# Kernel tuning notes

Measured on AMD Instinct MI355X. Metric: run time of the kernel, lower is better.

The kernel has to match this reference:

```python
import jax, jax.numpy as jnp
import numpy as np

B, S, E = 2, 2048, 1024
N_HEADS = 16
HEAD_DIM = E // N_HEADS  # 64
ATTN_SCALE = 1.0 / np.sqrt(E)  # NOTE: original scales by 1/sqrt(hidden_dim_phi), not head_dim
ROPE_BASE = 10000.0


def _rope(t):
    # t: (B, H, S, D) with D = HEAD_DIM; interleaved-pair RoPE (torchtune-style)
    d = t.shape[-1]
    s = t.shape[-2]
    inv_freq = 1.0 / (ROPE_BASE ** (jnp.arange(0, d, 2, dtype=jnp.float32) / d))  # (D/2,)
    ang = jnp.arange(s, dtype=jnp.float32)[:, None] * inv_freq[None, :]  # (S, D/2)
    cos, sin = jnp.cos(ang), jnp.sin(ang)  # (S, D/2)
    tp = t.reshape(t.shape[:-1] + (d // 2, 2))
    te, to = tp[..., 0], tp[..., 1]  # (B,H,S,D/2)
    oe = te * cos - to * sin
    oo = te * sin + to * cos
    return jnp.stack([oe, oo], axis=-1).reshape(t.shape)


def setup_inputs() -> dict:
    key = jax.random.key(0)
    ks = jax.random.split(key, 5)
    std = 0.02
    return {
        "x": jax.random.normal(ks[0], (B, S, E), dtype=jnp.float32),
        "W_q": jax.random.normal(ks[1], (E, E), dtype=jnp.float32) * std,
        "W_k": jax.random.normal(ks[2], (E, E), dtype=jnp.float32) * std,
        "W_v": jax.random.normal(ks[3], (E, E), dtype=jnp.float32) * std,
        "W_o": jax.random.normal(ks[4], (E, E), dtype=jnp.float32) * std,
    }


def reference(x, W_q, W_k, W_v, W_o):
    b, s, e = x.shape
    hd = e // N_HEADS
    # projections -> (B, H, S, D)
    def proj(w):
        return (x @ w).reshape(b, s, N_HEADS, hd).transpose(0, 2, 1, 3)
    q = _rope(proj(W_q))
    k = _rope(proj(W_k))
    v = proj(W_v)
    scores = jnp.einsum('bhsd,bhtd->bhst', q, k) * ATTN_SCALE  # (B,H,S,S)
    causal = jnp.triu(jnp.ones((s, s), dtype=bool), k=1)
    scores = jnp.where(causal, -jnp.inf, scores)
    probs = jax.nn.softmax(scores, axis=-1)  # dropout is identity in eval mode
    out = jnp.einsum('bhst,bhtd->bhsd', probs, v)
    out = out.transpose(0, 2, 1, 3).reshape(b, s, e)
    return out @ W_o
```

## Files before the change

kernel.cpp:

```cpp
#include <hip/hip_runtime.h>
#include <hip/hip_bf16.h>

#define S_LEN 2048
#define E_DIM 1024
#define NH 16
#define HD 64
#define ATTN_SCALE 0.03125f
#define QSCALE_L2E 0.045084312f

typedef __attribute__((ext_vector_type(8))) short short8;
typedef __attribute__((ext_vector_type(8))) unsigned short ushort8;
typedef __attribute__((ext_vector_type(4))) unsigned short ushort4_t;
typedef __attribute__((ext_vector_type(4))) float f32x4;
typedef __attribute__((ext_vector_type(4))) float f4;
typedef __attribute__((ext_vector_type(2))) unsigned int uint2_t;

__device__ __forceinline__ float bf2f(unsigned short u) {
    unsigned int x = ((unsigned int)u) << 16;
    return __builtin_bit_cast(float, x);
}
__device__ __forceinline__ unsigned short f2bf(float f) {
    unsigned int x = __builtin_bit_cast(unsigned int, f);
    x += 0x7FFFu + ((x >> 16) & 1u);
    return (unsigned short)(x >> 16);
}
__device__ __forceinline__ void gload16(const unsigned short* g, unsigned short* l) {
    __builtin_amdgcn_global_load_lds(
        (__attribute__((address_space(1))) void*)g,
        (__attribute__((address_space(3))) void*)l, 16, 0, 0);
}

__global__ __launch_bounds__(256) void k_convert(const float* __restrict__ x,
                                                 unsigned short* __restrict__ xb) {
    size_t i = ((size_t)blockIdx.x * 256 + threadIdx.x) * 8;
    f4 a = *(const f4*)(x + i);
    f4 b = *(const f4*)(x + i + 4);
    ushort8 o;
    o[0] = f2bf(a[0]); o[1] = f2bf(a[1]); o[2] = f2bf(a[2]); o[3] = f2bf(a[3]);
    o[4] = f2bf(b[0]); o[5] = f2bf(b[1]); o[6] = f2bf(b[2]); o[7] = f2bf(b[3]);
    *(ushort8*)(xb + i) = o;
}

__global__ __launch_bounds__(256) void k_transw(const float* W0, const float* W1,
                                                const float* W2, const float* W3,
                                                unsigned short* T0, unsigned short* T1,
                                                unsigned short* T2, unsigned short* T3) {
    const float* W; unsigned short* T;
    switch (blockIdx.z) {
        case 0: W = W0; T = T0; break;
        case 1: W = W1; T = T1; break;
        case 2: W = W2; T = T2; break;
        default: W = W3; T = T3; break;
    }
    __shared__ float tile[32][33];
    int tx = threadIdx.x, ty = threadIdx.y;
    int bx = blockIdx.x * 32, by = blockIdx.y * 32;
#pragma unroll
    for (int i = 0; i < 4; i++)
        tile[ty + i * 8][tx] = W[(size_t)(by + ty + i * 8) * E_DIM + bx + tx];
    __syncthreads();
#pragma unroll
    for (int i = 0; i < 4; i++)
        T[(size_t)(bx + ty + i * 8) * E_DIM + by + tx] = f2bf(tile[tx][ty + i * 8]);
}

__global__ __launch_bounds__(256) void k_rope_table(float* __restrict__ cosT,
                                                    float* __restrict__ sinT) {
    int idx = blockIdx.x * 256 + threadIdx.x;
    int s = idx >> 5, j = idx & 31;
    float inv = expf(-(float)j * (9.210340371976184f / 32.f));
    float ang = (float)s * inv;
    cosT[idx] = cosf(ang);
    sinT[idx] = sinf(ang);
}

template <int BM, int BN, int NBN, bool QKV3>
__global__ __launch_bounds__(256, 3)
void k_gemmN(const unsigned short* __restrict__ A,
             const unsigned short* __restrict__ B,
             unsigned short* __restrict__ Qo,
             unsigned short* __restrict__ Ko,
             unsigned short* __restrict__ Vto,
             float* __restrict__ Fo,
             const float* __restrict__ cosT,
             const float* __restrict__ sinT) {
    constexpr int THREADS = 256;
    constexpr int WM = BM / 2, WN = BN / 2;
    constexpr int FM = WM / 16, FN = WN / 16;
    constexpr int NT = E_DIM / 64;
    constexpr int AR = BM * 8 / THREADS;
    constexpr int BR = BN * 8 / THREADS;
    constexpr int STG = AR + BR;
    constexpr int NWG = (4096 / BM) * NBN;
    __shared__ unsigned short Al[2][BM * 64];
    __shared__ unsigned short Bl[2][BN * 64];
    int tid = threadIdx.x, lane = tid & 63, wid = tid >> 6;
    int l15 = lane & 15, lg = lane >> 4;
    int wr = wid >> 1, wc = wid & 1;
    int orig = blockIdx.y * NBN + blockIdx.x;
    int wg = (orig & 7) * (NWG / 8) + (orig >> 3);
    int bm = wg / NBN, bn = wg % NBN;

    auto stage = [&](int buf, int k0) {
#pragma unroll
        for (int i = 0; i < AR; i++) {
            int r = i * (THREADS / 8) + wid * 8 + (lane >> 3);
            int cs = (lane & 7) ^ (r & 7);
            gload16(A + (size_t)(bm * BM + r) * E_DIM + k0 + cs * 8,
                    &Al[buf][i * (THREADS * 8) + wid * 512]);
        }
#pragma unroll
        for (int i = 0; i < BR; i++) {
            int r = i * (THREADS / 8) + wid * 8 + (lane >> 3);
            int cs = (lane & 7) ^ (r & 7);
            gload16(B + (size_t)(bn * BN + r) * E_DIM + k0 + cs * 8,
                    &Bl[buf][i * (THREADS * 8) + wid * 512]);
        }
    };

    f32x4 acc[FM][FN] = {};
    stage(0, 0);
    for (int t = 0; t < NT; t++) {
        int cur = t & 1;
        if (t + 1 < NT) {
            stage(cur ^ 1, (t + 1) * 64);
            asm volatile("s_waitcnt vmcnt(%0)" :: "n"(STG) : "memory");
        } else {
            asm volatile("s_waitcnt vmcnt(0)" ::: "memory");
        }
        __builtin_amdgcn_s_barrier();
        __builtin_amdgcn_sched_barrier(0);
#pragma unroll
        for (int ks = 0; ks < 2; ks++) {
            short8 af[FM], bfv[FN];
#pragma unroll
            for (int m = 0; m < FM; m++) {
                int r = wr * WM + m * 16 + l15;
                int gc = ks * 4 + lg;
                af[m] = *(const short8*)&Al[cur][r * 64 + ((gc ^ (r & 7)) << 3)];
            }
#pragma unroll
            for (int n = 0; n < FN; n++) {
                int r = wc * WN + n * 16 + l15;
                int gc = ks * 4 + lg;
                bfv[n] = *(const short8*)&Bl[cur][r * 64 + ((gc ^ (r & 7)) << 3)];
            }
            __builtin_amdgcn_s_setprio(1);
#pragma unroll
            for (int m = 0; m < FM; m++)
#pragma unroll
                for (int n = 0; n < FN; n++)
                    acc[m][n] = __builtin_amdgcn_mfma_f32_16x16x32_bf16(
                        af[m], bfv[n], acc[m][n], 0, 0, 0);
            __builtin_amdgcn_s_setprio(0);
        }
        __builtin_amdgcn_s_barrier();
    }
#pragma unroll
    for (int m = 0; m < FM; m++) {
        int r0 = bm * BM + wr * WM + m * 16 + lg * 4;
#pragma unroll
        for (int n = 0; n < FN; n++) {
            int colg = bn * BN + wc * WN + n * 16 + l15;
            if (QKV3) {
                int z = colg >> 10, c1 = colg & 1023;
                if (z == 2) {
                    int h = c1 >> 6, d = c1 & 63;
                    int bb = r0 >> 11, s = r0 & 2047;
                    ushort4_t p;
#pragma unroll
                    for (int r = 0; r < 4; r++) p[r] = f2bf(acc[m][n][r]);
                    *(ushort4_t*)(Vto + (((size_t)((bb * 16 + h) * 64 + d)) << 11) + s) = p;
                } else {
                    unsigned short* T = z ? Ko : Qo;
                    int dl = c1 & 63, j = dl >> 1;
                    float sgn = (dl & 1) ? 1.f : -1.f;
                    float scq = z ? 1.f : QSCALE_L2E;
#pragma unroll
                    for (int r = 0; r < 4; r++) {
                        int row = r0 + r, s = row & 2047;
                        float c = cosT[s * 32 + j], sn = sinT[s * 32 + j];
                        float v = acc[m][n][r];
                        float p = __shfl_xor(v, 1);
                        T[(size_t)row * E_DIM + c1] = f2bf((v * c + sgn * p * sn) * scq);
                    }
                }
            } else {
#pragma unroll
                for (int r = 0; r < 4; r++)
                    Fo[(size_t)(r0 + r) * E_DIM + colg] = acc[m][n][r];
            }
        }
    }
}

__global__ __launch_bounds__(256, 3) void k_attn(const unsigned short* __restrict__ Q,
                                                 const unsigned short* __restrict__ K,
                                                 const unsigned short* __restrict__ Vt,
                                                 unsigned short* __restrict__ O) {
    __shared__ unsigned short K_lds[2][64 * 64];
    __shared__ unsigned short V_lds[2][64 * 64];
    __shared__ unsigned short P_lds[4][16][72];
    int tid = threadIdx.x, lane = tid & 63, wid = tid >> 6;
    int l15 = lane & 15, lg = lane >> 4;
    int orig = blockIdx.y * 16 + blockIdx.x;
    int wg = (orig & 7) * 64 + (orig >> 3);
    int jp = wg & 15, bh = wg >> 4;
    int b = bh >> 4, h = bh & 15;
    const size_t base_qk = (size_t)b * S_LEN * E_DIM + (size_t)h * HD;
    const unsigned short* Vbh = Vt + ((size_t)(bh * 64) << 11);

    auto stageK = [&](int buf, int kt) {
#pragma unroll
        for (int i = 0; i < 2; i++) {
            int r = i * 32 + (tid >> 3);
            int cs = (tid & 7) ^ (r & 7);
            gload16(K + base_qk + (size_t)(kt * 64 + r) * E_DIM + cs * 8,
                    &K_lds[buf][i * 2048 + tid * 8]);
        }
    };
    auto stageV = [&](int buf, int kt) {
#pragma unroll
        for (int i = 0; i < 2; i++) {
            int r = i * 32 + (tid >> 3);
            int cs = (tid & 7) ^ (r & 7);
            gload16(Vbh + (size_t)r * 2048 + kt * 64 + cs * 8,
                    &V_lds[buf][i * 2048 + tid * 8]);
        }
    };

    for (int pass = 0; pass < 2; ++pass) {
        int qt = pass ? (31 - jp) : jp;
        const unsigned short* Qb = Q + base_qk + (size_t)(qt * 64 + wid * 16) * E_DIM;
        short8 bq[2];
#pragma unroll
        for (int s2 = 0; s2 < 2; s2++)
            bq[s2] = *(const short8*)(Qb + (size_t)l15 * E_DIM + s2 * 32 + lg * 8);
        f32x4 acc_o[4] = {};
        float m_i = -1e30f, l_i = 0.f;
        int q_glob = qt * 64 + wid * 16 + l15;
        int nkt = qt + 1;
        stageK(0, 0);
        stageV(0, 0);
        asm volatile("s_waitcnt vmcnt(0)" ::: "memory");
        __builtin_amdgcn_s_barrier();
        __builtin_amdgcn_sched_barrier(0);
        int cur = 0;
        for (int kt = 0; kt < nkt; ++kt) {
            if (kt + 1 < nkt) {
                stageK(cur ^ 1, kt + 1);
                stageV(cur ^ 1, kt + 1);
            }
            f32x4 acc_s[4] = {};
            __builtin_amdgcn_s_setprio(1);
#pragma unroll
            for (int mf = 0; mf < 4; mf++) {
                int rK = mf * 16 + l15;
#pragma unroll
                for (int s2 = 0; s2 < 2; s2++) {
                    int gc = s2 * 4 + lg;
                    short8 a = *(const short8*)
                        &K_lds[cur][rK * 64 + ((gc ^ (rK & 7)) << 3)];
                    acc_s[mf] = __builtin_amdgcn_mfma_f32_16x16x32_bf16(
                        a, bq[s2], acc_s[mf], 0, 0, 0);
                }
            }
            __builtin_amdgcn_s_setprio(0);
            float sv[16];
            float vmax = -1e30f;
            if (kt == nkt - 1) {
#pragma unroll
                for (int mf = 0; mf < 4; mf++)
#pragma unroll
                    for (int r = 0; r < 4; r++) {
                        int kg = kt * 64 + mf * 16 + lg * 4 + r;
                        float v = acc_s[mf][r];
                        if (kg > q_glob) v = -1e30f;
                        sv[mf * 4 + r] = v;
                        vmax = fmaxf(vmax, v);
                    }
            } else {
#pragma unroll
                for (int mf = 0; mf < 4; mf++)
#pragma unroll
                    for (int r = 0; r < 4; r++) {
                        float v = acc_s[mf][r];
                        sv[mf * 4 + r] = v;
                        vmax = fmaxf(vmax, v);
                    }
            }
            vmax = fmaxf(vmax, __shfl_xor(vmax, 16));
            vmax = fmaxf(vmax, __shfl_xor(vmax, 32));
            if (!__all(vmax - m_i <= 8.0f)) {
                float m_new = fmaxf(m_i, vmax);
                float corr = exp2f(m_i - m_new);
                l_i *= corr;
#pragma unroll
                for (int r = 0; r < 4; r++) {
                    float c4 = __shfl(corr, lg * 4 + r);
#pragma unroll
                    for (int nf = 0; nf < 4; nf++) acc_o[nf][r] *= c4;
                }
                m_i = m_new;
            }
            float rowsum = 0.f;
#pragma unroll
            for (int i = 0; i < 16; i++) {
                float p = exp2f(sv[i] - m_i);
                sv[i] = p;
                rowsum += p;
            }
            rowsum += __shfl_xor(rowsum, 16);
            rowsum += __shfl_xor(rowsum, 32);
            l_i += rowsum;
#pragma unroll
            for (int mf = 0; mf < 4; mf++) {
                unsigned int w0, w1;
                asm("v_cvt_pk_bf16_f32 %0, %1, %2"
                    : "=v"(w0) : "v"(sv[mf * 4 + 0]), "v"(sv[mf * 4 + 1]));
                asm("v_cvt_pk_bf16_f32 %0, %1, %2"
                    : "=v"(w1) : "v"(sv[mf * 4 + 2]), "v"(sv[mf * 4 + 3]));
                uint2_t w; w[0] = w0; w[1] = w1;
                *(uint2_t*)&P_lds[wid][l15][mf * 16 + lg * 4] = w;
            }
            __builtin_amdgcn_s_setprio(1);
#pragma unroll
            for (int s2 = 0; s2 < 2; s2++) {
                short8 pa = *(const short8*)&P_lds[wid][l15][s2 * 32 + lg * 8];
#pragma unroll
                for (int nf = 0; nf < 4; nf++) {
                    int rV = nf * 16 + l15;
                    int gc = s2 * 4 + lg;
                    short8 bv = *(const short8*)
                        &V_lds[cur][rV * 64 + ((gc ^ (rV & 7)) << 3)];
                    acc_o[nf] = __builtin_amdgcn_mfma_f32_16x16x32_bf16(
                        pa, bv, acc_o[nf], 0, 0, 0);
                }
            }
            __builtin_amdgcn_s_setprio(0);
            asm volatile("s_waitcnt vmcnt(0)" ::: "memory");
            __builtin_amdgcn_s_barrier();
            __builtin_amdgcn_sched_barrier(0);
            cur ^= 1;
        }
        unsigned short* Ob = O + base_qk + (size_t)(qt * 64 + wid * 16) * E_DIM;
#pragma unroll
        for (int r = 0; r < 4; r++) {
            float linv = 1.f / __shfl(l_i, lg * 4 + r);
#pragma unroll
            for (int nf = 0; nf < 4; nf++)
                Ob[(size_t)(lg * 4 + r) * E_DIM + nf * 16 + l15] =
                    f2bf(acc_o[nf][r] * linv);
        }
    }
}

extern "C" void kernel_launch(void* const* d_in, const int* in_sizes, int n_in,
                              void* d_out, int out_size, void* d_ws, size_t ws_size,
                              hipStream_t stream) {
    (void)in_sizes; (void)n_in; (void)out_size; (void)ws_size;
    const float* x  = (const float*)d_in[0];
    const float* Wq = (const float*)d_in[1];
    const float* Wk = (const float*)d_in[2];
    const float* Wv = (const float*)d_in[3];
    const float* Wo = (const float*)d_in[4];

    unsigned short* us = (unsigned short*)d_ws;
    unsigned short* xb    = us;
    unsigned short* WqkvT = us + 4194304;
    unsigned short* WoT   = us + 7340032;
    unsigned short* Qb    = us + 8388608;
    unsigned short* Kb    = us + 12582912;
    unsigned short* Vt    = us + 16777216;
    unsigned short* AO    = us + 20971520;
    float* cosT = (float*)((char*)d_ws + 50331648);
    float* sinT = cosT + 65536;

    k_convert<<<2048, 256, 0, stream>>>(x, xb);
    k_transw<<<dim3(32, 32, 4), dim3(32, 8), 0, stream>>>(
        Wq, Wk, Wv, Wo, WqkvT, WqkvT + 1048576, WqkvT + 2097152, WoT);
    k_rope_table<<<256, 256, 0, stream>>>(cosT, sinT);
    k_gemmN<128, 64, 48, true><<<dim3(48, 32), 256, 0, stream>>>(
        xb, WqkvT, Qb, Kb, Vt, nullptr, cosT, sinT);
    k_attn<<<dim3(16, 32), 256, 0, stream>>>(Qb, Kb, Vt, AO);
    k_gemmN<128, 64, 16, false><<<dim3(16, 32), 256, 0, stream>>>(
        AO, WoT, nullptr, nullptr, nullptr, (float*)d_out, cosT, sinT);
}
```

Measured before the change: 117.5 us.

## Shrink attention blocks to 32 query rows and triple-buffer K/V loads

The attention kernel now uses 128-thread workgroups that each cover 32 query rows per pass, doubling the grid to 1024 blocks so causal work is spread more evenly and more blocks can be resident. K/V staging moves from double to triple buffering, prefetching two tiles ahead with partial vmcnt waits instead of draining all loads every iteration. The trade-off is that each K/V tile is now loaded by half as many threads and reused by fewer query rows, which raises global/L2 traffic per unit of compute, and more LDS is needed per block.

```diff
diff --git a/kernel.cpp b/kernel.cpp
--- a/kernel.cpp
+++ b/kernel.cpp
@@ -194,62 +194,69 @@
     }
 }
 
-__global__ __launch_bounds__(256, 3) void k_attn(const unsigned short* __restrict__ Q,
+__global__ __launch_bounds__(128, 2) void k_attn(const unsigned short* __restrict__ Q,
                                                  const unsigned short* __restrict__ K,
                                                  const unsigned short* __restrict__ Vt,
                                                  unsigned short* __restrict__ O) {
-    __shared__ unsigned short K_lds[2][64 * 64];
-    __shared__ unsigned short V_lds[2][64 * 64];
-    __shared__ unsigned short P_lds[4][16][72];
+    __shared__ unsigned short K_lds[3][64 * 64];
+    __shared__ unsigned short V_lds[3][64 * 64];
+    __shared__ unsigned short P_lds[2][16][72];
     int tid = threadIdx.x, lane = tid & 63, wid = tid >> 6;
     int l15 = lane & 15, lg = lane >> 4;
-    int orig = blockIdx.y * 16 + blockIdx.x;
-    int wg = (orig & 7) * 64 + (orig >> 3);
-    int jp = wg & 15, bh = wg >> 4;
+    int orig = blockIdx.y * 32 + blockIdx.x;
+    int wg = (orig & 7) * 128 + (orig >> 3);
+    int jp = wg & 31, bh = wg >> 5;
     int b = bh >> 4, h = bh & 15;
     const size_t base_qk = (size_t)b * S_LEN * E_DIM + (size_t)h * HD;
     const unsigned short* Vbh = Vt + ((size_t)(bh * 64) << 11);
 
     auto stageK = [&](int buf, int kt) {
 #pragma unroll
-        for (int i = 0; i < 2; i++) {
-            int r = i * 32 + (tid >> 3);
-            int cs = (tid & 7) ^ (r & 7);
+        for (int i = 0; i < 4; i++) {
+            int r = i * 16 + wid * 8 + (lane >> 3);
+            int cs = (lane & 7) ^ (r & 7);
             gload16(K + base_qk + (size_t)(kt * 64 + r) * E_DIM + cs * 8,
-                    &K_lds[buf][i * 2048 + tid * 8]);
+                    &K_lds[buf][i * 1024 + wid * 512]);
         }
     };
     auto stageV = [&](int buf, int kt) {
 #pragma unroll
-        for (int i = 0; i < 2; i++) {
-            int r = i * 32 + (tid >> 3);
-            int cs = (tid & 7) ^ (r & 7);
+        for (int i = 0; i < 4; i++) {
+            int r = i * 16 + wid * 8 + (lane >> 3);
+            int cs = (lane & 7) ^ (r & 7);
             gload16(Vbh + (size_t)r * 2048 + kt * 64 + cs * 8,
-                    &V_lds[buf][i * 2048 + tid * 8]);
+                    &V_lds[buf][i * 1024 + wid * 512]);
         }
     };
 
     for (int pass = 0; pass < 2; ++pass) {
-        int qt = pass ? (31 - jp) : jp;
-        const unsigned short* Qb = Q + base_qk + (size_t)(qt * 64 + wid * 16) * E_DIM;
+        int p = pass ? (63 - jp) : jp;
+        const unsigned short* Qb = Q + base_qk + (size_t)(p * 32 + wid * 16) * E_DIM;
         short8 bq[2];
 #pragma unroll
         for (int s2 = 0; s2 < 2; s2++)
             bq[s2] = *(const short8*)(Qb + (size_t)l15 * E_DIM + s2 * 32 + lg * 8);
         f32x4 acc_o[4] = {};
         float m_i = -1e30f, l_i = 0.f;
-        int q_glob = qt * 64 + wid * 16 + l15;
-        int nkt = qt + 1;
+        int q_glob = p * 32 + wid * 16 + l15;
+        int nkt = (p + 2) >> 1;
+        __builtin_amdgcn_s_barrier();
         stageK(0, 0);
         stageV(0, 0);
-        asm volatile("s_waitcnt vmcnt(0)" ::: "memory");
+        if (nkt > 1) {
+            stageK(1, 1);
+            stageV(1, 1);
+            asm volatile("s_waitcnt vmcnt(8)" ::: "memory");
+        } else {
+            asm volatile("s_waitcnt vmcnt(0)" ::: "memory");
+        }
         __builtin_amdgcn_s_barrier();
         __builtin_amdgcn_sched_barrier(0);
-        int cur = 0;
         for (int kt = 0; kt < nkt; ++kt) {
-            if (kt + 1 < nkt) {
-                stageK(cur ^ 1, kt + 1);
-                stageV(cur ^ 1, kt + 1);
+            int cur = kt % 3;
+            if (kt + 2 < nkt) {
+                stageK((kt + 2) % 3, kt + 2);
+                stageV((kt + 2) % 3, kt + 2);
             }
             f32x4 acc_s[4] = {};
             __builtin_amdgcn_s_setprio(1);
@@ -306,9 +313,9 @@
             float rowsum = 0.f;
 #pragma unroll
             for (int i = 0; i < 16; i++) {
-                float p = exp2f(sv[i] - m_i);
-                sv[i] = p;
-                rowsum += p;
+                float pv = exp2f(sv[i] - m_i);
+                sv[i] = pv;
+                rowsum += pv;
             }
             rowsum += __shfl_xor(rowsum, 16);
             rowsum += __shfl_xor(rowsum, 32);
@@ -338,12 +345,16 @@
                 }
             }
             __builtin_amdgcn_s_setprio(0);
-            asm volatile("s_waitcnt vmcnt(0)" ::: "memory");
-            __builtin_amdgcn_s_barrier();
-            __builtin_amdgcn_sched_barrier(0);
-            cur ^= 1;
-        }
-        unsigned short* Ob = O + base_qk + (size_t)(qt * 64 + wid * 16) * E_DIM;
+            if (kt + 1 < nkt) {
+                if (kt + 2 < nkt)
+                    asm volatile("s_waitcnt vmcnt(8)" ::: "memory");
+                else
+                    asm volatile("s_waitcnt vmcnt(0)" ::: "memory");
+                __builtin_amdgcn_s_barrier();
+                __builtin_amdgcn_sched_barrier(0);
+            }
+        }
+        unsigned short* Ob = O + base_qk + (size_t)(p * 32 + wid * 16) * E_DIM;
 #pragma unroll
         for (int r = 0; r < 4; r++) {
             float linv = 1.f / __shfl(l_i, lg * 4 + r);
@@ -382,7 +393,7 @@
     k_rope_table<<<256, 256, 0, stream>>>(cosT, sinT);
     k_gemmN<128, 64, 48, true><<<dim3(48, 32), 256, 0, stream>>>(
         xb, WqkvT, Qb, Kb, Vt, nullptr, cosT, sinT);
-    k_attn<<<dim3(16, 32), 256, 0, stream>>>(Qb, Kb, Vt, AO);
+    k_attn<<<dim3(32, 32), 128, 0, stream>>>(Qb, Kb, Vt, AO);
     k_gemmN<128, 64, 16, false><<<dim3(16, 32), 256, 0, stream>>>(
         AO, WoT, nullptr, nullptr, nullptr, (float*)d_out, cosT, sinT);
 }
```

Result: slower. 151.1 us (+28.6%).

## Rewrite attention with 32x32 MFMA tiles, register P shuffle, and XCD-aware scheduling

Applied to the files above, without the earlier changes.

The attention kernel now uses 2 waves per block, each owning 32 query rows, and runs 32x32x16 bf16 MFMAs instead of 16x16x32. The P matrix is handed from the S-MFMA layout to the PV-MFMA operand through cross-lane shuffles rather than an LDS round trip. Exp uses raw v_exp_f32 and the conditional rescale skip is dropped. Causal load balancing switches from pairing query tiles inside one block to one tile per block, mapped so each XCD handles a few heads with alternating tile order. Output is staged through LDS so global stores are coalesced. Smaller blocks with one tile each may load balance less evenly and reload K/V more often.

```diff
diff --git a/kernel.cpp b/kernel.cpp
--- a/kernel.cpp
+++ b/kernel.cpp
@@ -12,8 +12,9 @@
 typedef __attribute__((ext_vector_type(8))) unsigned short ushort8;
 typedef __attribute__((ext_vector_type(4))) unsigned short ushort4_t;
 typedef __attribute__((ext_vector_type(4))) float f32x4;
+typedef __attribute__((ext_vector_type(16))) float f32x16;
 typedef __attribute__((ext_vector_type(4))) float f4;
-typedef __attribute__((ext_vector_type(2))) unsigned int uint2_t;
+typedef __attribute__((ext_vector_type(4))) unsigned int uint4v;
 
 __device__ __forceinline__ float bf2f(unsigned short u) {
     unsigned int x = ((unsigned int)u) << 16;
@@ -23,6 +24,11 @@
     unsigned int x = __builtin_bit_cast(unsigned int, f);
     x += 0x7FFFu + ((x >> 16) & 1u);
     return (unsigned short)(x >> 16);
+}
+__device__ __forceinline__ float exp2_fast(float x) {
+    float r;
+    asm("v_exp_f32 %0, %1" : "=v"(r) : "v"(x));
+    return r;
 }
 __device__ __forceinline__ void gload16(const unsigned short* g, unsigned short* l) {
     __builtin_amdgcn_global_load_lds(
@@ -194,164 +200,165 @@
     }
 }
 
-__global__ __launch_bounds__(256, 3) void k_attn(const unsigned short* __restrict__ Q,
-                                                 const unsigned short* __restrict__ K,
-                                                 const unsigned short* __restrict__ Vt,
-                                                 unsigned short* __restrict__ O) {
-    __shared__ unsigned short K_lds[2][64 * 64];
-    __shared__ unsigned short V_lds[2][64 * 64];
-    __shared__ unsigned short P_lds[4][16][72];
+__global__ __launch_bounds__(128, 2)
+void k_attn32(const unsigned short* __restrict__ Q,
+              const unsigned short* __restrict__ K,
+              const unsigned short* __restrict__ Vt,
+              unsigned short* __restrict__ O) {
+    __shared__ unsigned short K_lds[2][4096];
+    __shared__ unsigned short V_lds[2][4096];
     int tid = threadIdx.x, lane = tid & 63, wid = tid >> 6;
-    int l15 = lane & 15, lg = lane >> 4;
-    int orig = blockIdx.y * 16 + blockIdx.x;
-    int wg = (orig & 7) * 64 + (orig >> 3);
-    int jp = wg & 15, bh = wg >> 4;
+    int l31 = lane & 31, hi = lane >> 5;
+    int orig = blockIdx.y * 32 + blockIdx.x;
+    int xcd = orig & 7, idx = orig >> 3;
+    int u = idx & 31, v = idx >> 5;
+    int bh = xcd * 4 + v;
+    int p = (v & 1) ? (31 - u) : u;
     int b = bh >> 4, h = bh & 15;
     const size_t base_qk = (size_t)b * S_LEN * E_DIM + (size_t)h * HD;
     const unsigned short* Vbh = Vt + ((size_t)(bh * 64) << 11);
 
     auto stageK = [&](int buf, int kt) {
 #pragma unroll
-        for (int i = 0; i < 2; i++) {
-            int r = i * 32 + (tid >> 3);
+        for (int i = 0; i < 4; i++) {
+            int r = i * 16 + (tid >> 3);
             int cs = (tid & 7) ^ (r & 7);
             gload16(K + base_qk + (size_t)(kt * 64 + r) * E_DIM + cs * 8,
-                    &K_lds[buf][i * 2048 + tid * 8]);
+                    &K_lds[buf][i * 1024 + tid * 8]);
         }
     };
     auto stageV = [&](int buf, int kt) {
 #pragma unroll
-        for (int i = 0; i < 2; i++) {
-            int r = i * 32 + (tid >> 3);
+        for (int i = 0; i < 4; i++) {
+            int r = i * 16 + (tid >> 3);
             int cs = (tid & 7) ^ (r & 7);
             gload16(Vbh + (size_t)r * 2048 + kt * 64 + cs * 8,
-                    &V_lds[buf][i * 2048 + tid * 8]);
+                    &V_lds[buf][i * 1024 + tid * 8]);
         }
     };
 
-    for (int pass = 0; pass < 2; ++pass) {
-        int qt = pass ? (31 - jp) : jp;
-        const unsigned short* Qb = Q + base_qk + (size_t)(qt * 64 + wid * 16) * E_DIM;
-        short8 bq[2];
-#pragma unroll
-        for (int s2 = 0; s2 < 2; s2++)
-            bq[s2] = *(const short8*)(Qb + (size_t)l15 * E_DIM + s2 * 32 + lg * 8);
-        f32x4 acc_o[4] = {};
-        float m_i = -1e30f, l_i = 0.f;
-        int q_glob = qt * 64 + wid * 16 + l15;
-        int nkt = qt + 1;
-        stageK(0, 0);
-        stageV(0, 0);
+    int q_glob = p * 64 + wid * 32 + l31;
+    const unsigned short* Qb = Q + base_qk + (size_t)q_glob * E_DIM;
+    short8 qf[4];
+#pragma unroll
+    for (int s = 0; s < 4; s++)
+        qf[s] = *(const short8*)(Qb + s * 16 + hi * 8);
+
+    f32x16 ot0 = {}, ot1 = {};
+    float m_i = -1e30f, l_i = 0.f;
+    int nkt = p + 1;
+    int swz = l31 & 7;
+    stageK(0, 0);
+    stageV(0, 0);
+    asm volatile("s_waitcnt vmcnt(0)" ::: "memory");
+    __builtin_amdgcn_s_barrier();
+    __builtin_amdgcn_sched_barrier(0);
+    int cur = 0;
+    for (int kt = 0; kt < nkt; ++kt) {
+        if (kt + 1 < nkt) {
+            stageK(cur ^ 1, kt + 1);
+            stageV(cur ^ 1, kt + 1);
+        }
+        f32x16 st0 = {}, st1 = {};
+        __builtin_amdgcn_s_setprio(1);
+#pragma unroll
+        for (int s = 0; s < 4; s++) {
+            int c = ((s * 2 + hi) ^ swz) << 3;
+            short8 ka0 = *(const short8*)&K_lds[cur][l31 * 64 + c];
+            short8 ka1 = *(const short8*)&K_lds[cur][(32 + l31) * 64 + c];
+            st0 = __builtin_amdgcn_mfma_f32_32x32x16_bf16(ka0, qf[s], st0, 0, 0, 0);
+            st1 = __builtin_amdgcn_mfma_f32_32x32x16_bf16(ka1, qf[s], st1, 0, 0, 0);
+        }
+        __builtin_amdgcn_s_setprio(0);
+        float p0[16], p1[16];
+        float vmax = -1e30f;
+        if (kt == nkt - 1) {
+#pragma unroll
+            for (int r = 0; r < 16; r++) {
+                int kg = kt * 64 + (r & 3) + 8 * (r >> 2) + 4 * hi;
+                float v0 = (kg > q_glob) ? -1e30f : st0[r];
+                float v1 = (kg + 32 > q_glob) ? -1e30f : st1[r];
+                p0[r] = v0; p1[r] = v1;
+                vmax = fmaxf(vmax, fmaxf(v0, v1));
+            }
+        } else {
+#pragma unroll
+            for (int r = 0; r < 16; r++) {
+                p0[r] = st0[r]; p1[r] = st1[r];
+                vmax = fmaxf(vmax, fmaxf(st0[r], st1[r]));
+            }
+        }
+        vmax = fmaxf(vmax, __shfl_xor(vmax, 32));
+        float m_new = fmaxf(m_i, vmax);
+        float corr = exp2_fast(m_i - m_new);
+        float rs = 0.f;
+#pragma unroll
+        for (int r = 0; r < 16; r++) {
+            p0[r] = exp2_fast(p0[r] - m_new);
+            p1[r] = exp2_fast(p1[r] - m_new);
+            rs += p0[r] + p1[r];
+        }
+        rs += __shfl_xor(rs, 32);
+        l_i = l_i * corr + rs;
+        m_i = m_new;
+#pragma unroll
+        for (int r = 0; r < 16; r++) { ot0[r] *= corr; ot1[r] *= corr; }
+        unsigned int pk0[8], pk1[8];
+#pragma unroll
+        for (int i = 0; i < 8; i++) {
+            asm("v_cvt_pk_bf16_f32 %0, %1, %2"
+                : "=v"(pk0[i]) : "v"(p0[2 * i]), "v"(p0[2 * i + 1]));
+            asm("v_cvt_pk_bf16_f32 %0, %1, %2"
+                : "=v"(pk1[i]) : "v"(p1[2 * i]), "v"(p1[2 * i + 1]));
+        }
+        bool ishi = hi != 0;
+        __builtin_amdgcn_s_setprio(1);
+#pragma unroll
+        for (int kk = 0; kk < 4; kk++) {
+            const unsigned int* pkt = (kk & 2) ? pk1 : pk0;
+            int off = (kk & 1) * 4;
+            unsigned int a  = pkt[off + 0], b2 = pkt[off + 1];
+            unsigned int c2 = pkt[off + 2], d2 = pkt[off + 3];
+            unsigned int sa = __shfl_xor(a, 32),  sb = __shfl_xor(b2, 32);
+            unsigned int sc = __shfl_xor(c2, 32), sd = __shfl_xor(d2, 32);
+            uint4v w;
+            w[0] = ishi ? sc : a;  w[1] = ishi ? sd : b2;
+            w[2] = ishi ? c2 : sa; w[3] = ishi ? d2 : sb;
+            short8 pf = __builtin_bit_cast(short8, w);
+            int cv = ((kk * 2 + hi) ^ swz) << 3;
+            short8 va0 = *(const short8*)&V_lds[cur][l31 * 64 + cv];
+            short8 va1 = *(const short8*)&V_lds[cur][(32 + l31) * 64 + cv];
+            ot0 = __builtin_amdgcn_mfma_f32_32x32x16_bf16(va0, pf, ot0, 0, 0, 0);
+            ot1 = __builtin_amdgcn_mfma_f32_32x32x16_bf16(va1, pf, ot1, 0, 0, 0);
+        }
+        __builtin_amdgcn_s_setprio(0);
         asm volatile("s_waitcnt vmcnt(0)" ::: "memory");
         __builtin_amdgcn_s_barrier();
         __builtin_amdgcn_sched_barrier(0);
-        int cur = 0;
-        for (int kt = 0; kt < nkt; ++kt) {
-            if (kt + 1 < nkt) {
-                stageK(cur ^ 1, kt + 1);
-                stageV(cur ^ 1, kt + 1);
-            }
-            f32x4 acc_s[4] = {};
-            __builtin_amdgcn_s_setprio(1);
-#pragma unroll
-            for (int mf = 0; mf < 4; mf++) {
-                int rK = mf * 16 + l15;
-#pragma unroll
-                for (int s2 = 0; s2 < 2; s2++) {
-                    int gc = s2 * 4 + lg;
-                    short8 a = *(const short8*)
-                        &K_lds[cur][rK * 64 + ((gc ^ (rK & 7)) << 3)];
-                    acc_s[mf] = __builtin_amdgcn_mfma_f32_16x16x32_bf16(
-                        a, bq[s2], acc_s[mf], 0, 0, 0);
-                }
-            }
-            __builtin_amdgcn_s_setprio(0);
-            float sv[16];
-            float vmax = -1e30f;
-            if (kt == nkt - 1) {
-#pragma unroll
-                for (int mf = 0; mf < 4; mf++)
-#pragma unroll
-                    for (int r = 0; r < 4; r++) {
-                        int kg = kt * 64 + mf * 16 + lg * 4 + r;
-                        float v = acc_s[mf][r];
-                        if (kg > q_glob) v = -1e30f;
-                        sv[mf * 4 + r] = v;
-                        vmax = fmaxf(vmax, v);
-                    }
-            } else {
-#pragma unroll
-                for (int mf = 0; mf < 4; mf++)
-#pragma unroll
-                    for (int r = 0; r < 4; r++) {
-                        float v = acc_s[mf][r];
-                        sv[mf * 4 + r] = v;
-                        vmax = fmaxf(vmax, v);
-                    }
-            }
-            vmax = fmaxf(vmax, __shfl_xor(vmax, 16));
-            vmax = fmaxf(vmax, __shfl_xor(vmax, 32));
-            if (!__all(vmax - m_i <= 8.0f)) {
-                float m_new = fmaxf(m_i, vmax);
-                float corr = exp2f(m_i - m_new);
-                l_i *= corr;
-#pragma unroll
-                for (int r = 0; r < 4; r++) {
-                    float c4 = __shfl(corr, lg * 4 + r);
-#pragma unroll
-                    for (int nf = 0; nf < 4; nf++) acc_o[nf][r] *= c4;
-                }
-                m_i = m_new;
-            }
-            float rowsum = 0.f;
-#pragma unroll
-            for (int i = 0; i < 16; i++) {
-                float p = exp2f(sv[i] - m_i);
-                sv[i] = p;
-                rowsum += p;
-            }
-            rowsum += __shfl_xor(rowsum, 16);
-            rowsum += __shfl_xor(rowsum, 32);
-            l_i += rowsum;
-#pragma unroll
-            for (int mf = 0; mf < 4; mf++) {
-                unsigned int w0, w1;
-                asm("v_cvt_pk_bf16_f32 %0, %1, %2"
-                    : "=v"(w0) : "v"(sv[mf * 4 + 0]), "v"(sv[mf * 4 + 1]));
-                asm("v_cvt_pk_bf16_f32 %0, %1, %2"
-                    : "=v"(w1) : "v"(sv[mf * 4 + 2]), "v"(sv[mf * 4 + 3]));
-                uint2_t w; w[0] = w0; w[1] = w1;
-                *(uint2_t*)&P_lds[wid][l15][mf * 16 + lg * 4] = w;
-            }
-            __builtin_amdgcn_s_setprio(1);
-#pragma unroll
-            for (int s2 = 0; s2 < 2; s2++) {
-                short8 pa = *(const short8*)&P_lds[wid][l15][s2 * 32 + lg * 8];
-#pragma unroll
-                for (int nf = 0; nf < 4; nf++) {
-                    int rV = nf * 16 + l15;
-                    int gc = s2 * 4 + lg;
-                    short8 bv = *(const short8*)
-                        &V_lds[cur][rV * 64 + ((gc ^ (rV & 7)) << 3)];
-                    acc_o[nf] = __builtin_amdgcn_mfma_f32_16x16x32_bf16(
-                        pa, bv, acc_o[nf], 0, 0, 0);
-                }
-            }
-            __builtin_amdgcn_s_setprio(0);
-            asm volatile("s_waitcnt vmcnt(0)" ::: "memory");
-            __builtin_amdgcn_s_barrier();
-            __builtin_amdgcn_sched_barrier(0);
-            cur ^= 1;
-        }
-        unsigned short* Ob = O + base_qk + (size_t)(qt * 64 + wid * 16) * E_DIM;
-#pragma unroll
-        for (int r = 0; r < 4; r++) {
-            float linv = 1.f / __shfl(l_i, lg * 4 + r);
-#pragma unroll
-            for (int nf = 0; nf < 4; nf++)
-                Ob[(size_t)(lg * 4 + r) * E_DIM + nf * 16 + l15] =
-                    f2bf(acc_o[nf][r] * linv);
-        }
+        cur ^= 1;
+    }
+    __builtin_amdgcn_s_barrier();
+    float linv = 1.f / l_i;
+    unsigned short* scb = &K_lds[0][0] + wid * 2304;
+#pragma unroll
+    for (int i = 0; i < 8; i++) {
+        int d = 2 * (i & 1) + 8 * (i >> 1) + 4 * hi;
+        unsigned int w0, w1;
+        float a0 = ot0[2 * i] * linv, a1 = ot0[2 * i + 1] * linv;
+        float b0 = ot1[2 * i] * linv, b1 = ot1[2 * i + 1] * linv;
+        asm("v_cvt_pk_bf16_f32 %0, %1, %2" : "=v"(w0) : "v"(a0), "v"(a1));
+        asm("v_cvt_pk_bf16_f32 %0, %1, %2" : "=v"(w1) : "v"(b0), "v"(b1));
+        *(unsigned int*)&scb[l31 * 72 + d] = w0;
+        *(unsigned int*)&scb[l31 * 72 + 32 + d] = w1;
+    }
+    asm volatile("s_waitcnt lgkmcnt(0)" ::: "memory");
+    __builtin_amdgcn_sched_barrier(0);
+    int qr = lane >> 1, half = (lane & 1) * 32;
+    unsigned short* Ob = O + base_qk + (size_t)(p * 64 + wid * 32 + qr) * E_DIM;
+#pragma unroll
+    for (int j = 0; j < 4; j++) {
+        short8 vv = *(const short8*)&scb[qr * 72 + half + j * 8];
+        *(short8*)(Ob + half + j * 8) = vv;
     }
 }
 
@@ -382,7 +389,7 @@
     k_rope_table<<<256, 256, 0, stream>>>(cosT, sinT);
     k_gemmN<128, 64, 48, true><<<dim3(48, 32), 256, 0, stream>>>(
         xb, WqkvT, Qb, Kb, Vt, nullptr, cosT, sinT);
-    k_attn<<<dim3(16, 32), 256, 0, stream>>>(Qb, Kb, Vt, AO);
+    k_attn32<<<dim3(32, 32), 128, 0, stream>>>(Qb, Kb, Vt, AO);
     k_gemmN<128, 64, 16, false><<<dim3(16, 32), 256, 0, stream>>>(
         AO, WoT, nullptr, nullptr, nullptr, (float*)d_out, cosT, sinT);
 }
```

Measured after the change: 117.7 us. Within noise of the previous version (+0.1%).
